# Optimization experiments

Hardware: AMD Instinct MI355X
Metric: run time of the kernel (lower is better)

## Reference

```python
import jax, jax.numpy as jnp
import numpy as np
from jax import lax

SCALES = [0.5, 0.25, 0.125, 0.0625]
D_MODEL = 256
IN_CH = 1


def setup_inputs() -> dict:
    key = jax.random.key(0)
    ks = jax.random.split(key, 16)
    x = jax.random.normal(ks[0], (2, D_MODEL, 256, 256), dtype=jnp.float32)
    m = jax.random.uniform(ks[1], (2, IN_CH, 256, 256), dtype=jnp.float32)
    s = 0.05
    Wq = jax.random.normal(ks[2], (D_MODEL, D_MODEL, 1, 1), jnp.float32) * s
    bq = jax.random.normal(ks[3], (D_MODEL,), jnp.float32) * s
    Wk = jax.random.normal(ks[4], (D_MODEL, D_MODEL, 1, 1), jnp.float32) * s
    bk = jax.random.normal(ks[5], (D_MODEL,), jnp.float32) * s
    Wv = jax.random.normal(ks[6], (D_MODEL, D_MODEL, 1, 1), jnp.float32) * s
    bv = jax.random.normal(ks[7], (D_MODEL,), jnp.float32) * s
    Wmq = jax.random.normal(ks[8], (D_MODEL, IN_CH, 1, 1), jnp.float32) * s
    bmq = jax.random.normal(ks[9], (D_MODEL,), jnp.float32) * s
    Wmk = jax.random.normal(ks[10], (D_MODEL, IN_CH, 1, 1), jnp.float32) * s
    bmk = jax.random.normal(ks[11], (D_MODEL,), jnp.float32) * s
    Wo = jax.random.normal(ks[12], (D_MODEL, D_MODEL, 3, 3), jnp.float32) * s
    bo = jax.random.normal(ks[13], (D_MODEL,), jnp.float32) * s
    return {"x": x, "m": m, "Wq": Wq, "bq": bq, "Wk": Wk, "bk": bk,
            "Wv": Wv, "bv": bv, "Wmq": Wmq, "bmq": bmq, "Wmk": Wmk, "bmk": bmk,
            "Wo": Wo, "bo": bo, "b": 1, "c": 256}


def _conv1x1(z, W, bias):
    # W: (O, I, 1, 1)
    return jnp.einsum('bihw,oi->bohw', z, W[:, :, 0, 0]) + bias[None, :, None, None]


def _forward(x, m, Wq, bq, Wk, bk, Wv, bv, Wmq, bmq, Wmk, bmk, Wo, bo, b, c):
    bt, _, h, w = x.shape  # h, w are multiples of 64 -> pad is zero
    t = bt // b
    n_scales = len(SCALES)
    d_k = c // n_scales

    q = _conv1x1(x, Wq, bq)
    k = _conv1x1(x, Wk, bk)
    v = _conv1x1(x, Wv, bv)
    mq = _conv1x1(m, Wmq, bmq)
    mk = _conv1x1(m, Wmk, bmk)

    outs = []
    for i, scale in enumerate(SCALES):
        height, width = int(h * scale), int(w * scale)
        out_h, out_w = h // height, w // width
        sl = slice(i * d_k, (i + 1) * d_k)

        def patch(z):
            # (b, t, d_k, out_h, height, out_w, width) -> (b, t*out_h*out_w, d_k*height*width)
            z = z[:, sl].reshape(b, t, d_k, out_h, height, out_w, width)
            z = z.transpose(0, 1, 3, 5, 2, 4, 6)
            return z.reshape(b, t * out_h * out_w, d_k * height * width)

        Q, K, V = patch(q), patch(k), patch(v)
        MQ, MK = patch(mq), patch(mk)
        inv_sqrt_d = 1.0 / jnp.sqrt(jnp.asarray(Q.shape[-1], jnp.float32))
        scores = jnp.einsum('bnd,bmd->bnm', Q, K) * inv_sqrt_d
        mask_scores = jnp.einsum('bnd,bmd->bnm', MQ, MK) * inv_sqrt_d
        p_attn = jax.nn.softmax(scores * mask_scores, axis=-1)
        y = jnp.einsum('bnm,bmd->bnd', p_attn, V)
        # back to (bt, d_k, h, w)
        y = y.reshape(b, t, out_h, out_w, d_k, height, width)
        y = y.transpose(0, 1, 4, 2, 5, 3, 6).reshape(bt, d_k, h, w)
        outs.append(y)

    out = jnp.concatenate(outs, axis=1)
    z = lax.conv_general_dilated(out, Wo, window_strides=(1, 1),
                                 padding=((1, 1), (1, 1)),
                                 dimension_numbers=('NCHW', 'OIHW', 'NCHW'))
    z = z + bo[None, :, None, None]
    return jnp.where(z > 0, z, 0.2 * z)  # LeakyReLU(0.2)


def reference(x, m, Wq, bq, Wk, bk, Wv, bv, Wmq, bmq, Wmk, bmk, Wo, bo, b, c):
    return _forward(x, m, Wq, bq, Wk, bk, Wv, bv, Wmq, bmq, Wmk, bmk, Wo, bo, b, c)
```

## Files before the change

kernel.cpp:

```cpp
#include <hip/hip_runtime.h>
#include <stdint.h>


typedef __attribute__((ext_vector_type(8))) short short8;
typedef __attribute__((ext_vector_type(4))) float floatx4;
typedef __attribute__((ext_vector_type(4))) unsigned int uintx4;

#define DEV static __device__ __forceinline__

DEV unsigned short f2bf(float f) {
  unsigned u = __builtin_bit_cast(unsigned, f);
  unsigned r = u + 0x7FFFu + ((u >> 16) & 1u);
  return (unsigned short)(r >> 16);
}

DEV void patch_row(int n, int sc, int lw, int& pt, int& sp0) {
  pt = n >> (2 + 2 * sc);
  int rem = n & ((4 << (2 * sc)) - 1);
  int oh = rem >> (1 + sc), ow = rem & ((2 << sc) - 1);
  sp0 = (oh << (lw + 8)) + (ow << lw);
}

__global__ void k_prep_w(const float* __restrict__ Wq, const float* __restrict__ Wk,
                         const float* __restrict__ Wv, const float* __restrict__ bq,
                         const float* __restrict__ bk, const float* __restrict__ bv,
                         const float* __restrict__ Wmq, const float* __restrict__ bmq,
                         const float* __restrict__ Wmk, const float* __restrict__ bmk,
                         unsigned short* __restrict__ wqkv, float* __restrict__ bias,
                         float* __restrict__ msc) {
  int b = blockIdx.x;
  int t = threadIdx.x;
  if (b < 768) {
    const float* src = b < 256 ? (Wq + b * 256) : (b < 512 ? (Wk + (b - 256) * 256)
                                                           : (Wv + (b - 512) * 256));
    wqkv[b * 256 + t] = f2bf(src[t]);
    if (t == 0) bias[b] = b < 256 ? bq[b] : (b < 512 ? bk[b - 256] : bv[b - 512]);
  } else {
    int sc = t >> 6, lane = t & 63;
    int ch = sc * 64 + lane;
    float a0 = Wmq[ch] * Wmk[ch];
    float a1 = Wmq[ch] * bmk[ch];
    float a2 = bmq[ch] * Wmk[ch];
    float a3 = bmq[ch] * bmk[ch];
    for (int off = 32; off; off >>= 1) {
      a0 += __shfl_xor(a0, off); a1 += __shfl_xor(a1, off);
      a2 += __shfl_xor(a2, off); a3 += __shfl_xor(a3, off);
    }
    if (lane == 0) {
      msc[sc * 4 + 0] = a0; msc[sc * 4 + 1] = a1;
      msc[sc * 4 + 2] = a2; msc[sc * 4 + 3] = a3;
    }
  }
}

__global__ void k_prep_wo(const float* __restrict__ Wo, unsigned short* __restrict__ wobf,
                          float* __restrict__ scoresG, unsigned int* __restrict__ pbuf) {
  int blk = blockIdx.x;
  if (blk < 2304) {
    int didx = blk >> 8, o = blk & 255, c = threadIdx.x;
    wobf[didx * 65536 + o * 256 + c] = f2bf(Wo[o * 2304 + c * 9 + didx]);
  } else {
    int i = (blk - 2304) * 256 + threadIdx.x;
    if (i < 559232) scoresG[i] = 0.f;
    if (i < 140032) pbuf[i] = 0u;
  }
}

__global__ __launch_bounds__(256) void k_xt(const float* __restrict__ x,
                                            unsigned short* __restrict__ xt) {
  __shared__ __align__(16) unsigned short tile[64][72];
  int p0 = blockIdx.x * 64, c0 = blockIdx.y * 64, t = blockIdx.z;
  int tid = threadIdx.x;
  {
    int cc = tid >> 2, pq = (tid & 3) * 16;
    const float* src = x + ((t * 256 + c0 + cc) * 65536 + p0 + pq);
    __align__(16) unsigned short tmp[16];
#pragma unroll
    for (int e = 0; e < 16; e += 4) {
      floatx4 v = *(const floatx4*)(src + e);
      tmp[e + 0] = f2bf(v[0]); tmp[e + 1] = f2bf(v[1]);
      tmp[e + 2] = f2bf(v[2]); tmp[e + 3] = f2bf(v[3]);
    }
    *(uintx4*)&tile[cc][pq] = *(const uintx4*)&tmp[0];
    *(uintx4*)&tile[cc][pq + 8] = *(const uintx4*)&tmp[8];
  }
  __syncthreads();
  {
    int pp = tid >> 2, cg = (tid & 3) * 16;
    __align__(16) unsigned short outv[16];
#pragma unroll
    for (int e = 0; e < 16; ++e) outv[e] = tile[cg + e][pp];
    unsigned short* dst = xt + ((t * 65536 + p0 + pp) * 256 + c0 + cg);
    *(uintx4*)dst = *(const uintx4*)&outv[0];
    *(uintx4*)(dst + 8) = *(const uintx4*)&outv[8];
  }
}

__global__ __launch_bounds__(256) void k_yt(const unsigned short* __restrict__ ynat,
                                            unsigned short* __restrict__ yt) {
  __shared__ __align__(16) unsigned short tile[64][72];
  int p0 = blockIdx.x * 64, c0 = blockIdx.y * 64, t = blockIdx.z;
  int tid = threadIdx.x;
  {
    int cc = tid >> 2, pq = (tid & 3) * 16;
    const unsigned short* src = ynat + ((t * 256 + c0 + cc) * 65536 + p0 + pq);
    *(uintx4*)&tile[cc][pq] = *(const uintx4*)src;
    *(uintx4*)&tile[cc][pq + 8] = *(const uintx4*)(src + 8);
  }
  __syncthreads();
  {
    int pp = tid >> 2, cg = (tid & 3) * 16;
    __align__(16) unsigned short outv[16];
#pragma unroll
    for (int e = 0; e < 16; ++e) outv[e] = tile[cg + e][pp];
    unsigned short* dst = yt + ((t * 65536 + p0 + pp) * 256 + c0 + cg);
    *(uintx4*)dst = *(const uintx4*)&outv[0];
    *(uintx4*)(dst + 8) = *(const uintx4*)&outv[8];
  }
}

__global__ __launch_bounds__(256, 2) void k_qkv(const unsigned short* __restrict__ xt,
                                                const unsigned short* __restrict__ wqkv,
                                                const float* __restrict__ bias,
                                                unsigned short* __restrict__ qkv) {
  extern __shared__ __align__(16) char smem[];
  auto As = (unsigned short (*)[64])(smem);
  auto Bs = (unsigned short (*)[64])(smem + 16384);
  auto Cs = (unsigned short (*)[280])(smem);
  int flat = blockIdx.x;
  int lg = (flat & 7) * 384 + (flat >> 3);
  int n_t = lg / 6, m_t = lg - n_t * 6;
  int n0 = n_t << 8, m0 = m_t << 7;
  int tid = threadIdx.x;
  int w = tid >> 6, l = tid & 63;
  int wr = w >> 1, wc = w & 1;
  int l15 = l & 15, lhi = l >> 4;
  int sr = tid >> 1, sbase = (tid & 1) * 4, r7 = sr & 7;
  int b7 = tid & 7;
  const unsigned short* gA = wqkv + (m0 + sr) * 256 + sbase * 8;
  const unsigned short* gB = xt + (n0 + tid) * 256;
  floatx4 zf = {0.f, 0.f, 0.f, 0.f};
  floatx4 acc[4][8];
#pragma unroll
  for (int i = 0; i < 4; ++i)
#pragma unroll
    for (int j = 0; j < 8; ++j) acc[i][j] = zf;
  uintx4 ra[4], rb[8];
#define QLOAD(K0) { const uintx4* pa = (const uintx4*)(gA + (K0)); \
                    ra[0] = pa[0]; ra[1] = pa[1]; ra[2] = pa[2]; ra[3] = pa[3]; \
                    const uintx4* pb = (const uintx4*)(gB + (K0)); \
                    rb[0] = pb[0]; rb[1] = pb[1]; rb[2] = pb[2]; rb[3] = pb[3]; \
                    rb[4] = pb[4]; rb[5] = pb[5]; rb[6] = pb[6]; rb[7] = pb[7]; }
  QLOAD(0);
#pragma unroll
  for (int ch = 0; ch < 4; ++ch) {
    __syncthreads();
#pragma unroll
    for (int j = 0; j < 4; ++j)
      *(uintx4*)&As[sr][((sbase + j) ^ r7) * 8] = ra[j];
#pragma unroll
    for (int j = 0; j < 8; ++j)
      *(uintx4*)&Bs[tid][(j ^ b7) * 8] = rb[j];
    __syncthreads();
    if (ch < 3) QLOAD((ch + 1) * 64);
#pragma unroll
    for (int kk = 0; kk < 2; ++kk) {
      short8 af[4];
#pragma unroll
      for (int f = 0; f < 4; ++f) {
        int arow = wr * 64 + f * 16 + l15;
        af[f] = *(const short8*)&As[arow][(((kk << 2) + lhi) ^ (arow & 7)) * 8];
      }
#pragma unroll
      for (int fn = 0; fn < 8; ++fn) {
        int brow = wc * 128 + fn * 16 + l15;
        short8 b = *(const short8*)&Bs[brow][(((kk << 2) + lhi) ^ (brow & 7)) * 8];
#pragma unroll
        for (int fm = 0; fm < 4; ++fm)
          acc[fm][fn] = __builtin_amdgcn_mfma_f32_16x16x32_bf16(af[fm], b, acc[fm][fn], 0, 0, 0);
      }
    }
  }
#undef QLOAD
#pragma unroll
  for (int h = 0; h < 2; ++h) {
    __syncthreads();
    if (wr == h) {
#pragma unroll
      for (int fm = 0; fm < 4; ++fm) {
#pragma unroll
        for (int rr = 0; rr < 4; ++rr) {
          int rl = fm * 16 + lhi * 4 + rr;
          float bv = bias[m0 + h * 64 + rl];
#pragma unroll
          for (int fn = 0; fn < 8; ++fn)
            Cs[rl][wc * 128 + fn * 16 + l15] = f2bf(acc[fm][fn][rr] + bv);
        }
      }
    }
    __syncthreads();
    {
      int p8 = (tid & 31) * 8;
      int pcol = n0 + p8;
      int t = pcol >> 16, p = pcol & 65535;
#pragma unroll
      for (int pass = 0; pass < 8; ++pass) {
        int rl = (tid >> 5) + pass * 8;
        uintx4 v = *(const uintx4*)&Cs[rl][p8];
        *(uintx4*)&qkv[((t * 768 + m0 + h * 64 + rl) << 16) + p] = v;
      }
    }
  }
}

__global__ __launch_bounds__(256) void k_gram2(const float* __restrict__ m,
                                               float* __restrict__ G) {
  __shared__ __align__(16) float Ns[32][68];
  __shared__ __align__(16) float Ms[32][68];
  int bid = blockIdx.x;
  int sc, tn, tm, z, nchunks, soff;
  if (bid < 32)      { sc = 0; tn = 0; tm = 0; z = bid;      nchunks = 8; soff = 0; }
  else if (bid < 40) { sc = 1; tn = 0; tm = 0; z = bid - 32; nchunks = 8; soff = 64; }
  else if (bid < 72) { int r = bid - 40; int tl = r >> 1; sc = 2; tn = tl >> 2; tm = tl & 3; z = r & 1; nchunks = 8; soff = 1088; }
  else               { int tl = bid - 72; sc = 3; tn = tl >> 4; tm = tl & 15; z = 0; nchunks = 4; soff = 17472; }
  int lw = 7 - sc, W = 1 << lw, N = 8 << (2 * sc);
  int kbase = z * nchunks * 64;
  int n0 = tn * 32, m0 = tm * 32;
  int tid = threadIdx.x;
  bool isA = tid < 128;
  int u = tid & 127;
  int srow = u >> 2, sslot0 = (u & 3) * 4;
  int grow = (isA ? n0 : m0) + srow;
  bool valid = grow < N;
  int pt = 0, sp0 = 0;
  if (valid) patch_row(grow, sc, lw, pt, sp0);
  int gbase = pt * 65536 + sp0;
  int trc = tid >> 4, tcc = tid & 15;
  float a00 = 0.f, a01 = 0.f, a10 = 0.f, a11 = 0.f;
  floatx4 zf = {0.f, 0.f, 0.f, 0.f};
  for (int c = 0; c < nchunks; ++c) {
    int k0 = kbase + c * 64;
    floatx4 v[4];
#pragma unroll
    for (int j = 0; j < 4; ++j) {
      v[j] = zf;
      if (valid) {
        int s = k0 + (sslot0 + j) * 4;
        int hh = s >> lw, ww = s & (W - 1);
        v[j] = *(const floatx4*)(m + gbase + (hh << 8) + ww);
      }
    }
    __syncthreads();
    float* dstrow = isA ? &Ns[srow][0] : &Ms[srow][0];
#pragma unroll
    for (int j = 0; j < 4; ++j) *(floatx4*)&dstrow[(sslot0 + j) * 4] = v[j];
    __syncthreads();
#pragma unroll 4
    for (int k = 0; k < 64; k += 4) {
      floatx4 na = *(const floatx4*)&Ns[2 * trc][k];
      floatx4 nb = *(const floatx4*)&Ns[2 * trc + 1][k];
      floatx4 ma = *(const floatx4*)&Ms[2 * tcc][k];
      floatx4 mb = *(const floatx4*)&Ms[2 * tcc + 1][k];
#pragma unroll
      for (int e = 0; e < 4; ++e) {
        a00 += na[e] * ma[e]; a01 += na[e] * mb[e];
        a10 += nb[e] * ma[e]; a11 += nb[e] * mb[e];
      }
    }
  }
  int rn = n0 + 2 * trc, rm = m0 + 2 * tcc;
  float res[2][2] = {{a00, a01}, {a10, a11}};
#pragma unroll
  for (int i = 0; i < 2; ++i)
#pragma unroll
    for (int j = 0; j < 2; ++j) {
      if (rn + i < N && rm + j < N) {
        float* dst = &G[soff + (rn + i) * N + rm + j];
        if (sc < 3) atomicAdd(dst, res[i][j]); else *dst = res[i][j];
      }
    }
}

__global__ void k_rsum(const float* __restrict__ m, float* __restrict__ rbuf) {
  int row = blockIdx.x, lane = threadIdx.x;
  int sc, n;
  if (row < 8)        { sc = 0; n = row; }
  else if (row < 40)  { sc = 1; n = row - 8; }
  else if (row < 168) { sc = 2; n = row - 40; }
  else                { sc = 3; n = row - 168; }
  int lw = 7 - sc, W = 1 << lw;
  int pt, sp0;
  patch_row(n, sc, lw, pt, sp0);
  int base = pt * 65536 + sp0;
  int S = 1 << (14 - 2 * sc);
  float acc = 0.f;
  for (int s = lane; s < S; s += 64) {
    int hh = s >> lw, ww = s & (W - 1);
    acc += m[base + (hh << 8) + ww];
  }
  for (int off = 32; off; off >>= 1) acc += __shfl_xor(acc, off);
  if (lane == 0) rbuf[row] = acc;
}

__global__ __launch_bounds__(256) void k_scores2(const unsigned short* __restrict__ qkv,
                                                 float* __restrict__ scores) {
  __shared__ __align__(16) unsigned short As[32][136];
  __shared__ __align__(16) unsigned short Bs[32][136];
  int bid = blockIdx.x;
  int sc, tn, tm, z, soff;
  if (bid < 256)      { sc = 0; tn = 0; tm = 0; z = bid;       soff = 0; }
  else                { sc = 1; tn = 0; tm = 0; z = bid - 256; soff = 64; }
  int lw = 7 - sc, W = 1 << lw, lS = 14 - 2 * sc, N = 8 << (2 * sc);
  int n0 = tn * 32, m0 = tm * 32;
  int kbase = z * 4096;
  int tid = threadIdx.x, w = tid >> 6, l = tid & 63;
  int wr = w >> 1, wc = w & 1, l15 = l & 15, lhi = l >> 4;
  floatx4 acc = {0.f, 0.f, 0.f, 0.f};
  bool isA = tid < 128;
  int u = tid & 127;
  int srow = u >> 2, sslot0 = (u & 3) * 4;
  int grow = (isA ? n0 : m0) + srow;
  int cb = (isA ? 0 : 256) + sc * 64;
  int pt = 0, sp0 = 0;
  bool valid = grow < N;
  if (valid) patch_row(grow, sc, lw, pt, sp0);
  int rowbase = (pt * 768 + cb) * 65536 + sp0;
  uintx4 zu = {0u, 0u, 0u, 0u};
  uintx4 r[4];
#define SLOAD(KS) { int kb2 = kbase + (KS) * 128; \
  _Pragma("unroll") for (int j = 0; j < 4; ++j) { \
    uintx4 v = zu; \
    if (valid) { int k = kb2 + (sslot0 + j) * 8; \
      int cl = k >> lS; int s = k & ((1 << lS) - 1); \
      int hh = s >> lw, ww = s & (W - 1); \
      v = *(const uintx4*)(qkv + rowbase + cl * 65536 + (hh << 8) + ww); } \
    r[j] = v; } }
  SLOAD(0);
  for (int ks = 0; ks < 32; ++ks) {
    __syncthreads();
    {
      unsigned short* dstrow = isA ? &As[srow][0] : &Bs[srow][0];
#pragma unroll
      for (int j = 0; j < 4; ++j) *(uintx4*)&dstrow[(sslot0 + j) * 8] = r[j];
    }
    __syncthreads();
    if (ks < 31) SLOAD(ks + 1);
#pragma unroll
    for (int kk = 0; kk < 4; ++kk) {
      short8 a = *(const short8*)&As[wr * 16 + l15][(kk * 4 + lhi) * 8];
      short8 b = *(const short8*)&Bs[wc * 16 + l15][(kk * 4 + lhi) * 8];
      acc = __builtin_amdgcn_mfma_f32_16x16x32_bf16(a, b, acc, 0, 0, 0);
    }
  }
#undef SLOAD
  int rrow = n0 + wr * 16 + lhi * 4;
  int ccol = m0 + wc * 16 + l15;
  if (ccol < N) {
#pragma unroll
    for (int rr = 0; rr < 4; ++rr)
      if (rrow + rr < N) atomicAdd(&scores[soff + (rrow + rr) * N + ccol], acc[rr]);
  }
}

__global__ __launch_bounds__(256) void k_scores_big(const unsigned short* __restrict__ qkv,
                                                    float* __restrict__ scores) {
  __shared__ __align__(16) unsigned short As[128][64];
  __shared__ __align__(16) unsigned short Bs[128][64];
  int flat = blockIdx.x;
  int lg = (flat & 7) * 20 + (flat >> 3);
  int sc, tn, tm, z, soff;
  if (lg < 32) { sc = 2; tn = 0; tm = 0; z = lg; soff = 1088; }
  else { int r = lg - 32; int tl = r >> 3; sc = 3; tn = tl >> 2; tm = tl & 3; z = r & 7; soff = 17472; }
  int N = 8 << (2 * sc);
  int lw = 7 - sc, W = 1 << lw, lS = 14 - 2 * sc;
  int n0 = tn * 128, m0 = tm * 128;
  int kbase = z * 2048;
  int tid = threadIdx.x;
  int w = tid >> 6, l = tid & 63;
  int wr = w >> 1, wc = w & 1;
  int l15 = l & 15, lhi = l >> 4;
  int sr = tid >> 1, sbase = (tid & 1) * 4, r7 = sr & 7;
  int ptA, spA, ptB, spB;
  patch_row(n0 + sr, sc, lw, ptA, spA);
  patch_row(m0 + sr, sc, lw, ptB, spB);
  int baseA = (ptA * 768 + sc * 64) * 65536 + spA;
  int baseB = (ptB * 768 + 256 + sc * 64) * 65536 + spB;
  floatx4 zf = {0.f, 0.f, 0.f, 0.f};
  floatx4 acc[4][4];
#pragma unroll
  for (int i = 0; i < 4; ++i)
#pragma unroll
    for (int j = 0; j < 4; ++j) acc[i][j] = zf;
  uintx4 ra[4], rb[4];
#define GLOAD(K0) { \
  _Pragma("unroll") for (int j = 0; j < 4; ++j) { \
    int k = kbase + (K0) + (sbase + j) * 8; \
    int cl = k >> lS; int s = k & ((1 << lS) - 1); \
    int hh = s >> lw, ww = s & (W - 1); \
    int off = cl * 65536 + (hh << 8) + ww; \
    ra[j] = *(const uintx4*)(qkv + baseA + off); \
    rb[j] = *(const uintx4*)(qkv + baseB + off); } }
  GLOAD(0);
  for (int st = 0; st < 32; ++st) {
    __syncthreads();
#pragma unroll
    for (int j = 0; j < 4; ++j) {
      *(uintx4*)&As[sr][((sbase + j) ^ r7) * 8] = ra[j];
      *(uintx4*)&Bs[sr][((sbase + j) ^ r7) * 8] = rb[j];
    }
    __syncthreads();
    if (st < 31) GLOAD((st + 1) * 64);
#pragma unroll
    for (int kk = 0; kk < 2; ++kk) {
      short8 af[4], bfr[4];
#pragma unroll
      for (int f = 0; f < 4; ++f) {
        int arow = wr * 64 + f * 16 + l15;
        af[f] = *(const short8*)&As[arow][(((kk << 2) + lhi) ^ (arow & 7)) * 8];
        int brow = wc * 64 + f * 16 + l15;
        bfr[f] = *(const short8*)&Bs[brow][(((kk << 2) + lhi) ^ (brow & 7)) * 8];
      }
#pragma unroll
      for (int fm = 0; fm < 4; ++fm)
#pragma unroll
        for (int fn = 0; fn < 4; ++fn)
          acc[fm][fn] = __builtin_amdgcn_mfma_f32_16x16x32_bf16(af[fm], bfr[fn], acc[fm][fn], 0, 0, 0);
    }
  }
#undef GLOAD
#pragma unroll
  for (int fm = 0; fm < 4; ++fm) {
    int nrow = n0 + wr * 64 + fm * 16 + lhi * 4;
#pragma unroll
    for (int rr = 0; rr < 4; ++rr) {
#pragma unroll
      for (int fn = 0; fn < 4; ++fn) {
        int mcol = m0 + wc * 64 + fn * 16 + l15;
        atomicAdd(&scores[soff + (nrow + rr) * N + mcol], acc[fm][fn][rr]);
      }
    }
  }
}

__global__ void k_softmax(const float* __restrict__ scores, const float* __restrict__ G,
                          const float* __restrict__ rbuf, const float* __restrict__ msc,
                          unsigned short* __restrict__ pbuf) {
  int row = blockIdx.x, lane = threadIdx.x;
  int sc, n, roff, soff, poff;
  if (row < 8)        { sc = 0; n = row;       roff = 0;   soff = 0;     poff = 0; }
  else if (row < 40)  { sc = 1; n = row - 8;   roff = 8;   soff = 64;    poff = 512; }
  else if (row < 168) { sc = 2; n = row - 40;  roff = 40;  soff = 1088;  poff = 1536; }
  else                { sc = 3; n = row - 168; roff = 168; soff = 17472; poff = 17920; }
  int N = 8 << (2 * sc);
  int Kpad = (sc < 2) ? 32 : N;
  float Sf = (float)(1 << (14 - 2 * sc));
  float invD = 1.0f / (float)(1 << (20 - 2 * sc));
  float alpha = msc[sc * 4 + 0], beta = msc[sc * 4 + 1];
  float gamma = msc[sc * 4 + 2], delta = msc[sc * 4 + 3];
  float rn = rbuf[roff + n];
  float vals[8];
  float mx = -1e30f;
#pragma unroll
  for (int j = 0; j < 8; ++j) {
    float v = -1e30f;
    int mcol = lane + j * 64;
    if (j * 64 < N && mcol < N) {
      float sq = scores[soff + n * N + mcol];
      float g = G[soff + n * N + mcol];
      float rm = rbuf[roff + mcol];
      v = sq * (alpha * g + beta * rn + gamma * rm + delta * Sf) * invD;
    }
    vals[j] = v;
    mx = fmaxf(mx, v);
  }
  for (int off = 32; off; off >>= 1) mx = fmaxf(mx, __shfl_xor(mx, off));
  float sum = 0.f;
#pragma unroll
  for (int j = 0; j < 8; ++j) {
    int mcol = lane + j * 64;
    float e = 0.f;
    if (j * 64 < N && mcol < N) e = __expf(vals[j] - mx);
    vals[j] = e;
    sum += e;
  }
  for (int off = 32; off; off >>= 1) sum += __shfl_xor(sum, off);
  float inv = 1.f / sum;
#pragma unroll
  for (int j = 0; j < 8; ++j) {
    int mcol = lane + j * 64;
    if (j * 64 < N && mcol < N) pbuf[poff + n * Kpad + mcol] = f2bf(vals[j] * inv);
  }
}

__global__ __launch_bounds__(256) void k_pv(const unsigned short* __restrict__ qkv,
                                            const unsigned short* __restrict__ pbuf,
                                            unsigned short* __restrict__ ynat) {
  int bid = blockIdx.x;
  int sc, bx, by;
  if (bid < 4096)      { sc = 0; bx = bid; by = 0; }
  else if (bid < 6144) { sc = 1; bx = bid - 4096; by = 0; }
  else if (bid < 8192) { int r = bid - 6144; sc = 2; bx = r >> 1; by = r & 1; }
  else                 { int r = bid - 8192; sc = 3; bx = r >> 3; by = r & 7; }
  int WR    = (sc == 0) ? 1 : (sc == 1) ? 2 : 4;
  int logWC = (sc == 0) ? 2 : (sc == 1) ? 1 : 0;
  int poff  = (sc == 0) ? 0 : (sc == 1) ? 512 : (sc == 2) ? 1536 : 17920;
  int lw = 7 - sc, W = 1 << lw;
  int lS = 14 - 2 * sc;
  int N = 8 << (2 * sc);
  int Kpad = (sc < 2) ? 32 : N;
  int WC = 1 << logWC;
  int d0 = bx * (WC * 64);
  int nb = by * (WR * 16);
  __shared__ __align__(16) unsigned short As[2][64][40];
  __shared__ __align__(16) unsigned short Bt[2][256][32];
  int tid = threadIdx.x;
  int w = tid >> 6, l = tid & 63;
  int wr = w >> logWC, wc = w & (WC - 1);
  int l15 = l & 15, lhi = l >> 4;
  floatx4 zf = {0.f, 0.f, 0.f, 0.f};
  floatx4 acc[4];
#pragma unroll
  for (int i = 0; i < 4; ++i) acc[i] = zf;
  int bmp = tid & 15;
  int dg = tid >> 4;
  bool act0 = (WC > 1) || (dg < 8);
  bool has1 = (WC == 4);
  bool doA = tid < WR * 64;
  int arow = tid >> 2, akg = (tid & 3) * 8;
  int ksteps = Kpad >> 5;
  uintx4 zu = {0u, 0u, 0u, 0u};
  int vcb = (512 + sc * 64) * 65536;
  uintx4 av = zu, lo0 = zu, hi0 = zu, lo1 = zu, hi1 = zu;
#define PLOADS(KS) { int k0 = (KS) * 32; \
    av = zu; lo0 = zu; hi0 = zu; lo1 = zu; hi1 = zu; \
    if (doA) av = *(const uintx4*)(pbuf + poff + (nb + arow) * Kpad + k0 + akg); \
    int gm0 = k0 + 2 * bmp, gm1 = gm0 + 1; \
    bool mv0 = gm0 < N, mv1 = gm1 < N; \
    int pt0 = 0, sp00 = 0, pt1 = 0, sp01 = 0; \
    if (mv0) patch_row(gm0, sc, lw, pt0, sp00); \
    if (mv1) patch_row(gm1, sc, lw, pt1, sp01); \
    { int d = d0 + dg * 8; int cl = d >> lS; int s = d & ((1 << lS) - 1); \
      int hh = s >> lw, ww = s & (W - 1); int sp = (hh << 8) + ww; \
      if (act0 && mv0) lo0 = *(const uintx4*)(qkv + pt0 * 768 * 65536 + vcb + cl * 65536 + sp00 + sp); \
      if (act0 && mv1) hi0 = *(const uintx4*)(qkv + pt1 * 768 * 65536 + vcb + cl * 65536 + sp01 + sp); } \
    if (has1) { int d = d0 + (dg + 16) * 8; int cl = d >> lS; int s = d & ((1 << lS) - 1); \
      int hh = s >> lw, ww = s & (W - 1); int sp = (hh << 8) + ww; \
      if (mv0) lo1 = *(const uintx4*)(qkv + pt0 * 768 * 65536 + vcb + cl * 65536 + sp00 + sp); \
      if (mv1) hi1 = *(const uintx4*)(qkv + pt1 * 768 * 65536 + vcb + cl * 65536 + sp01 + sp); } }
  PLOADS(0);
  for (int ks = 0; ks < ksteps; ++ks) {
    int b = ks & 1;
    if (doA) *(uintx4*)&As[b][arow][akg] = av;
    if (act0) {
      int du = dg * 8;
#pragma unroll
      for (int j = 0; j < 8; ++j) {
        int d = du + j;
        unsigned losh = (lo0[j >> 1] >> ((j & 1) * 16)) & 0xFFFFu;
        unsigned hish = (hi0[j >> 1] >> ((j & 1) * 16)) & 0xFFFFu;
        unsigned wv = losh | (hish << 16);
        int slot = (bmp >> 2) ^ ((d >> 1) & 3) ^ ((d >> 3) & 3);
        ((unsigned int*)&Bt[b][d][0])[slot * 4 + (bmp & 3)] = wv;
      }
    }
    if (has1) {
      int du = (dg + 16) * 8;
#pragma unroll
      for (int j = 0; j < 8; ++j) {
        int d = du + j;
        unsigned losh = (lo1[j >> 1] >> ((j & 1) * 16)) & 0xFFFFu;
        unsigned hish = (hi1[j >> 1] >> ((j & 1) * 16)) & 0xFFFFu;
        unsigned wv = losh | (hish << 16);
        int slot = (bmp >> 2) ^ ((d >> 1) & 3) ^ ((d >> 3) & 3);
        ((unsigned int*)&Bt[b][d][0])[slot * 4 + (bmp & 3)] = wv;
      }
    }
    __syncthreads();
    if (ks + 1 < ksteps) PLOADS(ks + 1);
    short8 a = *(const short8*)&As[b][wr * 16 + l15][lhi * 8];
#pragma unroll
    for (int fn = 0; fn < 4; ++fn) {
      int row = wc * 64 + fn * 16 + l15;
      int slot = lhi ^ ((row >> 1) & 3) ^ ((row >> 3) & 3);
      short8 bb = *(const short8*)&Bt[b][row][slot * 8];
      acc[fn] = __builtin_amdgcn_mfma_f32_16x16x32_bf16(a, bb, acc[fn], 0, 0, 0);
    }
  }
#undef PLOADS
  int nrow = nb + wr * 16 + lhi * 4;
#pragma unroll
  for (int rr = 0; rr < 4; ++rr) {
    int n = nrow + rr;
    if (n < N) {
      int pt, sp0;
      patch_row(n, sc, lw, pt, sp0);
#pragma unroll
      for (int fn = 0; fn < 4; ++fn) {
        int d = d0 + wc * 64 + fn * 16 + l15;
        int cl = d >> lS;
        int s = d & ((1 << lS) - 1);
        int hh = s >> lw, ww = s & (W - 1);
        int c = sc * 64 + cl;
        ynat[(pt * 256 + c) * 65536 + sp0 + (hh << 8) + ww] = f2bf(acc[fn][rr]);
      }
    }
  }
}

__global__ __launch_bounds__(256, 2) void k_conv(const unsigned short* __restrict__ yt,
                                                 const unsigned short* __restrict__ wo,
                                                 const float* __restrict__ bo,
                                                 float* __restrict__ out) {
  __shared__ __align__(16) unsigned short As[128][128];
  __shared__ __align__(16) unsigned short Bs[130][64];
  int flat = blockIdx.x;
  int lg = ((flat & 7) << 7) + (flat >> 3);
  int n_t = lg >> 1, m_t = lg & 1;
  int n0 = n_t << 8, m0 = m_t << 7;
  int tt = n0 >> 16, yy = (n0 >> 8) & 255;
  int tid = threadIdx.x;
  int w = tid >> 6, l = tid & 63;
  int wr = w >> 1, wc = w & 1;
  int l15 = l & 15, lhi = l >> 4;
  int a_d0 = tid >> 7, a_o0 = tid & 127;
  bool doA1 = tid < 128;
  bool doBh = tid >= 254;
  floatx4 zf = {0.f, 0.f, 0.f, 0.f};
  floatx4 acc[4][8];
#pragma unroll
  for (int i = 0; i < 4; ++i)
#pragma unroll
    for (int j = 0; j < 8; ++j) acc[i][j] = zf;
  uintx4 zu = {0u, 0u, 0u, 0u};
  uintx4 rb[4], ra0[4], ra1[4];
  const unsigned short* ybase = yt + (tt << 24);
#define CLOAD(ST) { \
    int dy = (ST) >> 3, cc = ((ST) & 7) << 5; \
    int yq = yy + dy - 1; \
    bool yv = (unsigned)yq < 256u; \
    { int xq = tid - 1; \
      if (yv && (unsigned)xq < 256u) { \
        const uintx4* p = (const uintx4*)(ybase + ((yq << 8) + xq) * 256 + cc); \
        rb[0] = p[0]; rb[1] = p[1]; rb[2] = p[2]; rb[3] = p[3]; \
      } else { rb[0] = zu; rb[1] = zu; rb[2] = zu; rb[3] = zu; } } \
    { const uintx4* p = (const uintx4*)(wo + (dy * 3 + a_d0) * 65536 + (m0 + a_o0) * 256 + cc); \
      ra0[0] = p[0]; ra0[1] = p[1]; ra0[2] = p[2]; ra0[3] = p[3]; } \
    if (doA1) { \
      const uintx4* p = (const uintx4*)(wo + (dy * 3 + 2) * 65536 + (m0 + tid) * 256 + cc); \
      ra1[0] = p[0]; ra1[1] = p[1]; ra1[2] = p[2]; ra1[3] = p[3]; \
    } else if (doBh) { \
      int xq = tid + 1; \
      if (yv && xq < 256) { \
        const uintx4* p = (const uintx4*)(ybase + ((yq << 8) + xq) * 256 + cc); \
        ra1[0] = p[0]; ra1[1] = p[1]; ra1[2] = p[2]; ra1[3] = p[3]; \
      } else { ra1[0] = zu; ra1[1] = zu; ra1[2] = zu; ra1[3] = zu; } } }
  CLOAD(0);
  for (int st = 0; st < 24; ++st) {
    __syncthreads();
    {
      int brow = tid >> 1, bhf = (tid & 1) * 4, br7 = brow & 7;
#pragma unroll
      for (int j = 0; j < 4; ++j)
        *(uintx4*)&Bs[brow][((bhf + j) ^ br7) * 8] = rb[j];
      int ao7 = a_o0 & 7;
#pragma unroll
      for (int j = 0; j < 4; ++j)
        *(uintx4*)&As[a_o0][((a_d0 * 4 + j) ^ ao7) * 8] = ra0[j];
      if (doA1) {
        int o7 = tid & 7;
#pragma unroll
        for (int j = 0; j < 4; ++j)
          *(uintx4*)&As[tid][((8 + j) ^ o7) * 8] = ra1[j];
      } else if (doBh) {
        int xh = tid + 2;
        int brow2 = xh >> 1, bhf2 = (xh & 1) * 4, br72 = brow2 & 7;
#pragma unroll
        for (int j = 0; j < 4; ++j)
          *(uintx4*)&Bs[brow2][((bhf2 + j) ^ br72) * 8] = ra1[j];
      }
    }
    __syncthreads();
    if (st < 23) CLOAD(st + 1);
#pragma unroll
    for (int dx = 0; dx < 3; ++dx) {
      short8 af[4];
#pragma unroll
      for (int f = 0; f < 4; ++f) {
        int ol = wr * 64 + f * 16 + l15;
        af[f] = *(const short8*)&As[ol][((dx * 4 + lhi) ^ (ol & 7)) * 8];
      }
#pragma unroll
      for (int fn = 0; fn < 8; ++fn) {
        int xh = wc * 128 + fn * 16 + l15 + dx;
        short8 b = *(const short8*)&Bs[xh >> 1][((((xh & 1) * 4 + lhi)) ^ ((xh >> 1) & 7)) * 8];
#pragma unroll
        for (int fm = 0; fm < 4; ++fm)
          acc[fm][fn] = __builtin_amdgcn_mfma_f32_16x16x32_bf16(af[fm], b, acc[fm][fn], 0, 0, 0);
      }
    }
  }
#undef CLOAD
#pragma unroll
  for (int fm = 0; fm < 4; ++fm) {
    int o = m0 + wr * 64 + fm * 16 + lhi * 4;
#pragma unroll
    for (int rr = 0; rr < 4; ++rr) {
      float bias = bo[o + rr];
#pragma unroll
      for (int fn = 0; fn < 8; ++fn) {
        int xcol = wc * 128 + fn * 16 + l15;
        float z = acc[fm][fn][rr] + bias;
        out[((tt * 256 + o + rr) << 16) + (yy << 8) + xcol] = z > 0.f ? z : 0.2f * z;
      }
    }
  }
}

extern "C" void kernel_launch(void* const* d_in, const int* in_sizes, int n_in,
                              void* d_out, int out_size, void* d_ws, size_t ws_size,
                              hipStream_t stream) {
  const float* x   = (const float*)d_in[0];
  const float* m   = (const float*)d_in[1];
  const float* Wq  = (const float*)d_in[2];
  const float* bq  = (const float*)d_in[3];
  const float* Wk  = (const float*)d_in[4];
  const float* bk  = (const float*)d_in[5];
  const float* Wv  = (const float*)d_in[6];
  const float* bv  = (const float*)d_in[7];
  const float* Wmq = (const float*)d_in[8];
  const float* bmq = (const float*)d_in[9];
  const float* Wmk = (const float*)d_in[10];
  const float* bmk = (const float*)d_in[11];
  const float* Wo  = (const float*)d_in[12];
  const float* bo  = (const float*)d_in[13];

  char* ws = (char*)d_ws;
  unsigned short* qkv   = (unsigned short*)(ws);
  unsigned short* xtb   = (unsigned short*)(ws + 201326592);
  unsigned short* wqkv  = (unsigned short*)(ws + 268435456);
  unsigned short* wobf  = (unsigned short*)(ws + 268828672);
  float* bias           = (float*)(ws + 270008320);
  float* msc            = (float*)(ws + 270011392);
  float* scores         = (float*)(ws + 270011456);
  float* G              = (float*)(ws + 271129920);
  float* rbuf           = (float*)(ws + 272248384);
  unsigned short* pbuf  = (unsigned short*)(ws + 272251104);
  float* out            = (float*)d_out;
  unsigned short* ynat  = (unsigned short*)d_out;

  k_prep_w<<<dim3(769), dim3(256), 0, stream>>>(Wq, Wk, Wv, bq, bk, bv, Wmq, bmq, Wmk, bmk,
                                                wqkv, bias, msc);
  k_prep_wo<<<dim3(4489), dim3(256), 0, stream>>>(Wo, wobf, scores, (unsigned int*)pbuf);
  k_xt<<<dim3(1024, 4, 2), dim3(256), 0, stream>>>(x, xtb);
  k_qkv<<<dim3(3072), dim3(256), 49152, stream>>>(xtb, wqkv, bias, qkv);
  k_gram2<<<dim3(328), dim3(256), 0, stream>>>(m, G);
  k_rsum<<<dim3(680), dim3(64), 0, stream>>>(m, rbuf);
  k_scores2<<<dim3(320), dim3(256), 0, stream>>>(qkv, scores);
  k_scores_big<<<dim3(160), dim3(256), 0, stream>>>(qkv, scores);
  k_softmax<<<dim3(680), dim3(64), 0, stream>>>(scores, G, rbuf, msc, pbuf);
  k_pv<<<dim3(10240), dim3(256), 0, stream>>>(qkv, pbuf, ynat);
  k_yt<<<dim3(1024, 4, 2), dim3(256), 0, stream>>>(ynat, xtb);
  k_conv<<<dim3(1024), dim3(256), 0, stream>>>(xtb, wobf, bo, out);
}
```

Baseline: 583.7 us.

## Merge small kernels and retile 3x3 conv to 64-channel blocks

Merges the two weight-prep kernels into one launch, the mask Gram and row-sum kernels into one, and the small and big score kernels into one. Each merge removes a launch and lets independent blocks run together. The 3x3 output conv now computes a 64-output-channel by 256-pixel tile per block instead of 128x256, with half the accumulators, smaller shared memory, a 3-blocks-per-SM bound and twice the blocks. This trades more occupancy for re-reading the activation tile once per extra channel block.

```diff
diff --git a/kernel.cpp b/kernel.cpp
--- a/kernel.cpp
+++ b/kernel.cpp
@@ -21,21 +21,25 @@
   sp0 = (oh << (lw + 8)) + (ow << lw);
 }
 
-__global__ void k_prep_w(const float* __restrict__ Wq, const float* __restrict__ Wk,
-                         const float* __restrict__ Wv, const float* __restrict__ bq,
-                         const float* __restrict__ bk, const float* __restrict__ bv,
-                         const float* __restrict__ Wmq, const float* __restrict__ bmq,
-                         const float* __restrict__ Wmk, const float* __restrict__ bmk,
-                         unsigned short* __restrict__ wqkv, float* __restrict__ bias,
-                         float* __restrict__ msc) {
-  int b = blockIdx.x;
+__global__ void k_prep(const float* __restrict__ Wq, const float* __restrict__ Wk,
+                       const float* __restrict__ Wv, const float* __restrict__ bq,
+                       const float* __restrict__ bk, const float* __restrict__ bv,
+                       const float* __restrict__ Wmq, const float* __restrict__ bmq,
+                       const float* __restrict__ Wmk, const float* __restrict__ bmk,
+                       const float* __restrict__ Wo, const float* __restrict__ bo,
+                       unsigned short* __restrict__ wqkv, float* __restrict__ bias,
+                       float* __restrict__ msc, unsigned short* __restrict__ wobf,
+                       float* __restrict__ scoresG, unsigned int* __restrict__ pbuf) {
+  int bid = blockIdx.x;
   int t = threadIdx.x;
-  if (b < 768) {
-    const float* src = b < 256 ? (Wq + b * 256) : (b < 512 ? (Wk + (b - 256) * 256)
-                                                           : (Wv + (b - 512) * 256));
-    wqkv[b * 256 + t] = f2bf(src[t]);
-    if (t == 0) bias[b] = b < 256 ? bq[b] : (b < 512 ? bk[b - 256] : bv[b - 512]);
-  } else {
+  if (bid < 768) {
+    const float* src = bid < 256 ? (Wq + bid * 256) : (bid < 512 ? (Wk + (bid - 256) * 256)
+                                                                 : (Wv + (bid - 512) * 256));
+    wqkv[bid * 256 + t] = f2bf(src[t]);
+    if (t == 0) bias[bid] = bid < 256 ? bq[bid] : (bid < 512 ? bk[bid - 256] : bv[bid - 512]);
+    return;
+  }
+  if (bid == 768) {
     int sc = t >> 6, lane = t & 63;
     int ch = sc * 64 + lane;
     float a0 = Wmq[ch] * Wmk[ch];
@@ -50,17 +54,14 @@
       msc[sc * 4 + 0] = a0; msc[sc * 4 + 1] = a1;
       msc[sc * 4 + 2] = a2; msc[sc * 4 + 3] = a3;
     }
-  }
-}
-
-__global__ void k_prep_wo(const float* __restrict__ Wo, unsigned short* __restrict__ wobf,
-                          float* __restrict__ scoresG, unsigned int* __restrict__ pbuf) {
-  int blk = blockIdx.x;
+    return;
+  }
+  int blk = bid - 769;
   if (blk < 2304) {
-    int didx = blk >> 8, o = blk & 255, c = threadIdx.x;
+    int didx = blk >> 8, o = blk & 255, c = t;
     wobf[didx * 65536 + o * 256 + c] = f2bf(Wo[o * 2304 + c * 9 + didx]);
   } else {
-    int i = (blk - 2304) * 256 + threadIdx.x;
+    int i = (blk - 2304) * 256 + t;
     if (i < 559232) scoresG[i] = 0.f;
     if (i < 140032) pbuf[i] = 0u;
   }
@@ -213,11 +214,37 @@
   }
 }
 
-__global__ __launch_bounds__(256) void k_gram2(const float* __restrict__ m,
-                                               float* __restrict__ G) {
+__global__ __launch_bounds__(256) void k_mask(const float* __restrict__ m,
+                                              float* __restrict__ G,
+                                              float* __restrict__ rbuf) {
+  int bid = blockIdx.x;
+  int tid = threadIdx.x;
+  if (bid >= 328) {
+    int row = (bid - 328) * 4 + (tid >> 6);
+    int lane = tid & 63;
+    if (row < 680) {
+      int sc, n;
+      if (row < 8)        { sc = 0; n = row; }
+      else if (row < 40)  { sc = 1; n = row - 8; }
+      else if (row < 168) { sc = 2; n = row - 40; }
+      else                { sc = 3; n = row - 168; }
+      int lw = 7 - sc, W = 1 << lw;
+      int pt, sp0;
+      patch_row(n, sc, lw, pt, sp0);
+      int base = pt * 65536 + sp0;
+      int S = 1 << (14 - 2 * sc);
+      float acc = 0.f;
+      for (int s = lane; s < S; s += 64) {
+        int hh = s >> lw, ww = s & (W - 1);
+        acc += m[base + (hh << 8) + ww];
+      }
+      for (int off = 32; off; off >>= 1) acc += __shfl_xor(acc, off);
+      if (lane == 0) rbuf[row] = acc;
+    }
+    return;
+  }
   __shared__ __align__(16) float Ns[32][68];
   __shared__ __align__(16) float Ms[32][68];
-  int bid = blockIdx.x;
   int sc, tn, tm, z, nchunks, soff;
   if (bid < 32)      { sc = 0; tn = 0; tm = 0; z = bid;      nchunks = 8; soff = 0; }
   else if (bid < 40) { sc = 1; tn = 0; tm = 0; z = bid - 32; nchunks = 8; soff = 64; }
@@ -226,7 +253,6 @@
   int lw = 7 - sc, W = 1 << lw, N = 8 << (2 * sc);
   int kbase = z * nchunks * 64;
   int n0 = tn * 32, m0 = tm * 32;
-  int tid = threadIdx.x;
   bool isA = tid < 128;
   int u = tid & 127;
   int srow = u >> 2, sslot0 = (u & 3) * 4;
@@ -281,52 +307,108 @@
     }
 }
 
-__global__ void k_rsum(const float* __restrict__ m, float* __restrict__ rbuf) {
-  int row = blockIdx.x, lane = threadIdx.x;
-  int sc, n;
-  if (row < 8)        { sc = 0; n = row; }
-  else if (row < 40)  { sc = 1; n = row - 8; }
-  else if (row < 168) { sc = 2; n = row - 40; }
-  else                { sc = 3; n = row - 168; }
-  int lw = 7 - sc, W = 1 << lw;
-  int pt, sp0;
-  patch_row(n, sc, lw, pt, sp0);
-  int base = pt * 65536 + sp0;
-  int S = 1 << (14 - 2 * sc);
-  float acc = 0.f;
-  for (int s = lane; s < S; s += 64) {
-    int hh = s >> lw, ww = s & (W - 1);
-    acc += m[base + (hh << 8) + ww];
-  }
-  for (int off = 32; off; off >>= 1) acc += __shfl_xor(acc, off);
-  if (lane == 0) rbuf[row] = acc;
-}
-
-__global__ __launch_bounds__(256) void k_scores2(const unsigned short* __restrict__ qkv,
-                                                 float* __restrict__ scores) {
-  __shared__ __align__(16) unsigned short As[32][136];
-  __shared__ __align__(16) unsigned short Bs[32][136];
+__global__ __launch_bounds__(256) void k_scores_all(const unsigned short* __restrict__ qkv,
+                                                    float* __restrict__ scores) {
+  __shared__ __align__(16) char sbuf[32768];
   int bid = blockIdx.x;
-  int sc, tn, tm, z, soff;
-  if (bid < 256)      { sc = 0; tn = 0; tm = 0; z = bid;       soff = 0; }
-  else                { sc = 1; tn = 0; tm = 0; z = bid - 256; soff = 64; }
-  int lw = 7 - sc, W = 1 << lw, lS = 14 - 2 * sc, N = 8 << (2 * sc);
-  int n0 = tn * 32, m0 = tm * 32;
-  int kbase = z * 4096;
-  int tid = threadIdx.x, w = tid >> 6, l = tid & 63;
+  int tid = threadIdx.x;
+  int w = tid >> 6, l = tid & 63;
   int wr = w >> 1, wc = w & 1, l15 = l & 15, lhi = l >> 4;
-  floatx4 acc = {0.f, 0.f, 0.f, 0.f};
-  bool isA = tid < 128;
-  int u = tid & 127;
-  int srow = u >> 2, sslot0 = (u & 3) * 4;
-  int grow = (isA ? n0 : m0) + srow;
-  int cb = (isA ? 0 : 256) + sc * 64;
-  int pt = 0, sp0 = 0;
-  bool valid = grow < N;
-  if (valid) patch_row(grow, sc, lw, pt, sp0);
-  int rowbase = (pt * 768 + cb) * 65536 + sp0;
   uintx4 zu = {0u, 0u, 0u, 0u};
-  uintx4 r[4];
+  floatx4 zf = {0.f, 0.f, 0.f, 0.f};
+  if (bid < 160) {
+    auto As = (unsigned short (*)[64])(sbuf);
+    auto Bs = (unsigned short (*)[64])(sbuf + 16384);
+    int lg = (bid & 7) * 20 + (bid >> 3);
+    int sc, tn, tm, z, soff;
+    if (lg < 32) { sc = 2; tn = 0; tm = 0; z = lg; soff = 1088; }
+    else { int r = lg - 32; int tl = r >> 3; sc = 3; tn = tl >> 2; tm = tl & 3; z = r & 7; soff = 17472; }
+    int N = 8 << (2 * sc);
+    int lw = 7 - sc, W = 1 << lw, lS = 14 - 2 * sc;
+    int n0 = tn * 128, m0 = tm * 128;
+    int kbase = z * 2048;
+    int sr = tid >> 1, sbase = (tid & 1) * 4, r7 = sr & 7;
+    int ptA, spA, ptB, spB;
+    patch_row(n0 + sr, sc, lw, ptA, spA);
+    patch_row(m0 + sr, sc, lw, ptB, spB);
+    int baseA = (ptA * 768 + sc * 64) * 65536 + spA;
+    int baseB = (ptB * 768 + 256 + sc * 64) * 65536 + spB;
+    floatx4 acc[4][4];
+#pragma unroll
+    for (int i = 0; i < 4; ++i)
+#pragma unroll
+      for (int j = 0; j < 4; ++j) acc[i][j] = zf;
+    uintx4 ra[4], rb[4];
+#define GLOAD(K0) { \
+  _Pragma("unroll") for (int j = 0; j < 4; ++j) { \
+    int k = kbase + (K0) + (sbase + j) * 8; \
+    int cl = k >> lS; int s = k & ((1 << lS) - 1); \
+    int hh = s >> lw, ww = s & (W - 1); \
+    int off = cl * 65536 + (hh << 8) + ww; \
+    ra[j] = *(const uintx4*)(qkv + baseA + off); \
+    rb[j] = *(const uintx4*)(qkv + baseB + off); } }
+    GLOAD(0);
+    for (int st = 0; st < 32; ++st) {
+      __syncthreads();
+#pragma unroll
+      for (int j = 0; j < 4; ++j) {
+        *(uintx4*)&As[sr][((sbase + j) ^ r7) * 8] = ra[j];
+        *(uintx4*)&Bs[sr][((sbase + j) ^ r7) * 8] = rb[j];
+      }
+      __syncthreads();
+      if (st < 31) GLOAD((st + 1) * 64);
+#pragma unroll
+      for (int kk = 0; kk < 2; ++kk) {
+        short8 af[4], bfr[4];
+#pragma unroll
+        for (int f = 0; f < 4; ++f) {
+          int arow = wr * 64 + f * 16 + l15;
+          af[f] = *(const short8*)&As[arow][(((kk << 2) + lhi) ^ (arow & 7)) * 8];
+          int brow = wc * 64 + f * 16 + l15;
+          bfr[f] = *(const short8*)&Bs[brow][(((kk << 2) + lhi) ^ (brow & 7)) * 8];
+        }
+#pragma unroll
+        for (int fm = 0; fm < 4; ++fm)
+#pragma unroll
+          for (int fn = 0; fn < 4; ++fn)
+            acc[fm][fn] = __builtin_amdgcn_mfma_f32_16x16x32_bf16(af[fm], bfr[fn], acc[fm][fn], 0, 0, 0);
+      }
+    }
+#undef GLOAD
+#pragma unroll
+    for (int fm = 0; fm < 4; ++fm) {
+      int nrow = n0 + wr * 64 + fm * 16 + lhi * 4;
+#pragma unroll
+      for (int rr = 0; rr < 4; ++rr) {
+#pragma unroll
+        for (int fn = 0; fn < 4; ++fn) {
+          int mcol = m0 + wc * 64 + fn * 16 + l15;
+          atomicAdd(&scores[soff + (nrow + rr) * N + mcol], acc[fm][fn][rr]);
+        }
+      }
+    }
+    return;
+  }
+  {
+    auto As = (unsigned short (*)[136])(sbuf);
+    auto Bs = (unsigned short (*)[136])(sbuf + 8704);
+    int b2 = bid - 160;
+    int sc, z, soff;
+    if (b2 < 256) { sc = 0; z = b2;       soff = 0; }
+    else          { sc = 1; z = b2 - 256; soff = 64; }
+    int lw = 7 - sc, W = 1 << lw, lS = 14 - 2 * sc, N = 8 << (2 * sc);
+    int kbase = z * 4096;
+    floatx4 acc = zf;
+    bool isA = tid < 128;
+    int u = tid & 127;
+    int srow = u >> 2, sslot0 = (u & 3) * 4;
+    int grow = srow;
+    int cb = (isA ? 0 : 256) + sc * 64;
+    int pt = 0, sp0 = 0;
+    bool valid = grow < N;
+    if (valid) patch_row(grow, sc, lw, pt, sp0);
+    int rowbase = (pt * 768 + cb) * 65536 + sp0;
+    uintx4 r[4];
 #define SLOAD(KS) { int kb2 = kbase + (KS) * 128; \
   _Pragma("unroll") for (int j = 0; j < 4; ++j) { \
     uintx4 v = zu; \
@@ -335,109 +417,30 @@
       int hh = s >> lw, ww = s & (W - 1); \
       v = *(const uintx4*)(qkv + rowbase + cl * 65536 + (hh << 8) + ww); } \
     r[j] = v; } }
-  SLOAD(0);
-  for (int ks = 0; ks < 32; ++ks) {
-    __syncthreads();
-    {
-      unsigned short* dstrow = isA ? &As[srow][0] : &Bs[srow][0];
-#pragma unroll
-      for (int j = 0; j < 4; ++j) *(uintx4*)&dstrow[(sslot0 + j) * 8] = r[j];
-    }
-    __syncthreads();
-    if (ks < 31) SLOAD(ks + 1);
-#pragma unroll
-    for (int kk = 0; kk < 4; ++kk) {
-      short8 a = *(const short8*)&As[wr * 16 + l15][(kk * 4 + lhi) * 8];
-      short8 b = *(const short8*)&Bs[wc * 16 + l15][(kk * 4 + lhi) * 8];
-      acc = __builtin_amdgcn_mfma_f32_16x16x32_bf16(a, b, acc, 0, 0, 0);
-    }
-  }
+    SLOAD(0);
+    for (int ks = 0; ks < 32; ++ks) {
+      __syncthreads();
+      {
+        unsigned short* dstrow = isA ? &As[srow][0] : &Bs[srow][0];
+#pragma unroll
+        for (int j = 0; j < 4; ++j) *(uintx4*)&dstrow[(sslot0 + j) * 8] = r[j];
+      }
+      __syncthreads();
+      if (ks < 31) SLOAD(ks + 1);
+#pragma unroll
+      for (int kk = 0; kk < 4; ++kk) {
+        short8 a = *(const short8*)&As[wr * 16 + l15][(kk * 4 + lhi) * 8];
+        short8 b = *(const short8*)&Bs[wc * 16 + l15][(kk * 4 + lhi) * 8];
+        acc = __builtin_amdgcn_mfma_f32_16x16x32_bf16(a, b, acc, 0, 0, 0);
+      }
+    }
 #undef SLOAD
-  int rrow = n0 + wr * 16 + lhi * 4;
-  int ccol = m0 + wc * 16 + l15;
-  if (ccol < N) {
-#pragma unroll
-    for (int rr = 0; rr < 4; ++rr)
-      if (rrow + rr < N) atomicAdd(&scores[soff + (rrow + rr) * N + ccol], acc[rr]);
-  }
-}
-
-__global__ __launch_bounds__(256) void k_scores_big(const unsigned short* __restrict__ qkv,
-                                                    float* __restrict__ scores) {
-  __shared__ __align__(16) unsigned short As[128][64];
-  __shared__ __align__(16) unsigned short Bs[128][64];
-  int flat = blockIdx.x;
-  int lg = (flat & 7) * 20 + (flat >> 3);
-  int sc, tn, tm, z, soff;
-  if (lg < 32) { sc = 2; tn = 0; tm = 0; z = lg; soff = 1088; }
-  else { int r = lg - 32; int tl = r >> 3; sc = 3; tn = tl >> 2; tm = tl & 3; z = r & 7; soff = 17472; }
-  int N = 8 << (2 * sc);
-  int lw = 7 - sc, W = 1 << lw, lS = 14 - 2 * sc;
-  int n0 = tn * 128, m0 = tm * 128;
-  int kbase = z * 2048;
-  int tid = threadIdx.x;
-  int w = tid >> 6, l = tid & 63;
-  int wr = w >> 1, wc = w & 1;
-  int l15 = l & 15, lhi = l >> 4;
-  int sr = tid >> 1, sbase = (tid & 1) * 4, r7 = sr & 7;
-  int ptA, spA, ptB, spB;
-  patch_row(n0 + sr, sc, lw, ptA, spA);
-  patch_row(m0 + sr, sc, lw, ptB, spB);
-  int baseA = (ptA * 768 + sc * 64) * 65536 + spA;
-  int baseB = (ptB * 768 + 256 + sc * 64) * 65536 + spB;
-  floatx4 zf = {0.f, 0.f, 0.f, 0.f};
-  floatx4 acc[4][4];
-#pragma unroll
-  for (int i = 0; i < 4; ++i)
-#pragma unroll
-    for (int j = 0; j < 4; ++j) acc[i][j] = zf;
-  uintx4 ra[4], rb[4];
-#define GLOAD(K0) { \
-  _Pragma("unroll") for (int j = 0; j < 4; ++j) { \
-    int k = kbase + (K0) + (sbase + j) * 8; \
-    int cl = k >> lS; int s = k & ((1 << lS) - 1); \
-    int hh = s >> lw, ww = s & (W - 1); \
-    int off = cl * 65536 + (hh << 8) + ww; \
-    ra[j] = *(const uintx4*)(qkv + baseA + off); \
-    rb[j] = *(const uintx4*)(qkv + baseB + off); } }
-  GLOAD(0);
-  for (int st = 0; st < 32; ++st) {
-    __syncthreads();
-#pragma unroll
-    for (int j = 0; j < 4; ++j) {
-      *(uintx4*)&As[sr][((sbase + j) ^ r7) * 8] = ra[j];
-      *(uintx4*)&Bs[sr][((sbase + j) ^ r7) * 8] = rb[j];
-    }
-    __syncthreads();
-    if (st < 31) GLOAD((st + 1) * 64);
-#pragma unroll
-    for (int kk = 0; kk < 2; ++kk) {
-      short8 af[4], bfr[4];
-#pragma unroll
-      for (int f = 0; f < 4; ++f) {
-        int arow = wr * 64 + f * 16 + l15;
-        af[f] = *(const short8*)&As[arow][(((kk << 2) + lhi) ^ (arow & 7)) * 8];
-        int brow = wc * 64 + f * 16 + l15;
-        bfr[f] = *(const short8*)&Bs[brow][(((kk << 2) + lhi) ^ (brow & 7)) * 8];
-      }
-#pragma unroll
-      for (int fm = 0; fm < 4; ++fm)
-#pragma unroll
-        for (int fn = 0; fn < 4; ++fn)
-          acc[fm][fn] = __builtin_amdgcn_mfma_f32_16x16x32_bf16(af[fm], bfr[fn], acc[fm][fn], 0, 0, 0);
-    }
-  }
-#undef GLOAD
-#pragma unroll
-  for (int fm = 0; fm < 4; ++fm) {
-    int nrow = n0 + wr * 64 + fm * 16 + lhi * 4;
-#pragma unroll
-    for (int rr = 0; rr < 4; ++rr) {
-#pragma unroll
-      for (int fn = 0; fn < 4; ++fn) {
-        int mcol = m0 + wc * 64 + fn * 16 + l15;
-        atomicAdd(&scores[soff + (nrow + rr) * N + mcol], acc[fm][fn][rr]);
-      }
+    int rrow = wr * 16 + lhi * 4;
+    int ccol = wc * 16 + l15;
+    if (ccol < N) {
+#pragma unroll
+      for (int rr = 0; rr < 4; ++rr)
+        if (rrow + rr < N) atomicAdd(&scores[soff + (rrow + rr) * N + ccol], acc[rr]);
     }
   }
 }
@@ -607,32 +610,31 @@
   }
 }
 
-__global__ __launch_bounds__(256, 2) void k_conv(const unsigned short* __restrict__ yt,
+__global__ __launch_bounds__(256, 3) void k_conv(const unsigned short* __restrict__ yt,
                                                  const unsigned short* __restrict__ wo,
                                                  const float* __restrict__ bo,
                                                  float* __restrict__ out) {
-  __shared__ __align__(16) unsigned short As[128][128];
+  __shared__ __align__(16) unsigned short As[64][128];
   __shared__ __align__(16) unsigned short Bs[130][64];
   int flat = blockIdx.x;
-  int lg = ((flat & 7) << 7) + (flat >> 3);
-  int n_t = lg >> 1, m_t = lg & 1;
-  int n0 = n_t << 8, m0 = m_t << 7;
+  int lg = ((flat & 7) << 8) + (flat >> 3);
+  int n_t = lg >> 2, m_t = lg & 3;
+  int n0 = n_t << 8, m0 = m_t << 6;
   int tt = n0 >> 16, yy = (n0 >> 8) & 255;
   int tid = threadIdx.x;
   int w = tid >> 6, l = tid & 63;
-  int wr = w >> 1, wc = w & 1;
   int l15 = l & 15, lhi = l >> 4;
-  int a_d0 = tid >> 7, a_o0 = tid & 127;
-  bool doA1 = tid < 128;
+  bool doA = tid < 192;
+  int a_dx = tid >> 6, a_o = tid & 63;
   bool doBh = tid >= 254;
   floatx4 zf = {0.f, 0.f, 0.f, 0.f};
-  floatx4 acc[4][8];
+  floatx4 acc[4][4];
 #pragma unroll
   for (int i = 0; i < 4; ++i)
 #pragma unroll
-    for (int j = 0; j < 8; ++j) acc[i][j] = zf;
+    for (int j = 0; j < 4; ++j) acc[i][j] = zf;
   uintx4 zu = {0u, 0u, 0u, 0u};
-  uintx4 rb[4], ra0[4], ra1[4];
+  uintx4 rb[4], ra[4], rh[4];
   const unsigned short* ybase = yt + (tt << 24);
 #define CLOAD(ST) { \
     int dy = (ST) >> 3, cc = ((ST) & 7) << 5; \
@@ -643,17 +645,15 @@
         const uintx4* p = (const uintx4*)(ybase + ((yq << 8) + xq) * 256 + cc); \
         rb[0] = p[0]; rb[1] = p[1]; rb[2] = p[2]; rb[3] = p[3]; \
       } else { rb[0] = zu; rb[1] = zu; rb[2] = zu; rb[3] = zu; } } \
-    { const uintx4* p = (const uintx4*)(wo + (dy * 3 + a_d0) * 65536 + (m0 + a_o0) * 256 + cc); \
-      ra0[0] = p[0]; ra0[1] = p[1]; ra0[2] = p[2]; ra0[3] = p[3]; } \
-    if (doA1) { \
-      const uintx4* p = (const uintx4*)(wo + (dy * 3 + 2) * 65536 + (m0 + tid) * 256 + cc); \
-      ra1[0] = p[0]; ra1[1] = p[1]; ra1[2] = p[2]; ra1[3] = p[3]; \
+    if (doA) { \
+      const uintx4* p = (const uintx4*)(wo + (dy * 3 + a_dx) * 65536 + (m0 + a_o) * 256 + cc); \
+      ra[0] = p[0]; ra[1] = p[1]; ra[2] = p[2]; ra[3] = p[3]; \
     } else if (doBh) { \
-      int xq = tid + 1; \
+      int xq = tid + 1;   \
       if (yv && xq < 256) { \
         const uintx4* p = (const uintx4*)(ybase + ((yq << 8) + xq) * 256 + cc); \
-        ra1[0] = p[0]; ra1[1] = p[1]; ra1[2] = p[2]; ra1[3] = p[3]; \
-      } else { ra1[0] = zu; ra1[1] = zu; ra1[2] = zu; ra1[3] = zu; } } }
+        rh[0] = p[0]; rh[1] = p[1]; rh[2] = p[2]; rh[3] = p[3]; \
+      } else { rh[0] = zu; rh[1] = zu; rh[2] = zu; rh[3] = zu; } } }
   CLOAD(0);
   for (int st = 0; st < 24; ++st) {
     __syncthreads();
@@ -662,21 +662,17 @@
 #pragma unroll
       for (int j = 0; j < 4; ++j)
         *(uintx4*)&Bs[brow][((bhf + j) ^ br7) * 8] = rb[j];
-      int ao7 = a_o0 & 7;
-#pragma unroll
-      for (int j = 0; j < 4; ++j)
-        *(uintx4*)&As[a_o0][((a_d0 * 4 + j) ^ ao7) * 8] = ra0[j];
-      if (doA1) {
-        int o7 = tid & 7;
+      if (doA) {
+        int o7 = a_o & 7;
 #pragma unroll
         for (int j = 0; j < 4; ++j)
-          *(uintx4*)&As[tid][((8 + j) ^ o7) * 8] = ra1[j];
+          *(uintx4*)&As[a_o][((a_dx * 4 + j) ^ o7) * 8] = ra[j];
       } else if (doBh) {
         int xh = tid + 2;
         int brow2 = xh >> 1, bhf2 = (xh & 1) * 4, br72 = brow2 & 7;
 #pragma unroll
         for (int j = 0; j < 4; ++j)
-          *(uintx4*)&Bs[brow2][((bhf2 + j) ^ br72) * 8] = ra1[j];
+          *(uintx4*)&Bs[brow2][((bhf2 + j) ^ br72) * 8] = rh[j];
       }
     }
     __syncthreads();
@@ -686,12 +682,12 @@
       short8 af[4];
 #pragma unroll
       for (int f = 0; f < 4; ++f) {
-        int ol = wr * 64 + f * 16 + l15;
+        int ol = f * 16 + l15;
         af[f] = *(const short8*)&As[ol][((dx * 4 + lhi) ^ (ol & 7)) * 8];
       }
 #pragma unroll
-      for (int fn = 0; fn < 8; ++fn) {
-        int xh = wc * 128 + fn * 16 + l15 + dx;
+      for (int fn = 0; fn < 4; ++fn) {
+        int xh = w * 64 + fn * 16 + l15 + dx;
         short8 b = *(const short8*)&Bs[xh >> 1][((((xh & 1) * 4 + lhi)) ^ ((xh >> 1) & 7)) * 8];
 #pragma unroll
         for (int fm = 0; fm < 4; ++fm)
@@ -702,13 +698,13 @@
 #undef CLOAD
 #pragma unroll
   for (int fm = 0; fm < 4; ++fm) {
-    int o = m0 + wr * 64 + fm * 16 + lhi * 4;
+    int o = m0 + fm * 16 + lhi * 4;
 #pragma unroll
     for (int rr = 0; rr < 4; ++rr) {
       float bias = bo[o + rr];
 #pragma unroll
-      for (int fn = 0; fn < 8; ++fn) {
-        int xcol = wc * 128 + fn * 16 + l15;
+      for (int fn = 0; fn < 4; ++fn) {
+        int xcol = w * 64 + fn * 16 + l15;
         float z = acc[fm][fn][rr] + bias;
         out[((tt * 256 + o + rr) << 16) + (yy << 8) + xcol] = z > 0.f ? z : 0.2f * z;
       }
@@ -748,17 +744,15 @@
   float* out            = (float*)d_out;
   unsigned short* ynat  = (unsigned short*)d_out;
 
-  k_prep_w<<<dim3(769), dim3(256), 0, stream>>>(Wq, Wk, Wv, bq, bk, bv, Wmq, bmq, Wmk, bmk,
-                                                wqkv, bias, msc);
-  k_prep_wo<<<dim3(4489), dim3(256), 0, stream>>>(Wo, wobf, scores, (unsigned int*)pbuf);
+  k_prep<<<dim3(5258), dim3(256), 0, stream>>>(Wq, Wk, Wv, bq, bk, bv, Wmq, bmq, Wmk, bmk,
+                                               Wo, bo, wqkv, bias, msc, wobf, scores,
+                                               (unsigned int*)pbuf);
   k_xt<<<dim3(1024, 4, 2), dim3(256), 0, stream>>>(x, xtb);
   k_qkv<<<dim3(3072), dim3(256), 49152, stream>>>(xtb, wqkv, bias, qkv);
-  k_gram2<<<dim3(328), dim3(256), 0, stream>>>(m, G);
-  k_rsum<<<dim3(680), dim3(64), 0, stream>>>(m, rbuf);
-  k_scores2<<<dim3(320), dim3(256), 0, stream>>>(qkv, scores);
-  k_scores_big<<<dim3(160), dim3(256), 0, stream>>>(qkv, scores);
+  k_mask<<<dim3(498), dim3(256), 0, stream>>>(m, G, rbuf);
+  k_scores_all<<<dim3(480), dim3(256), 0, stream>>>(qkv, scores);
   k_softmax<<<dim3(680), dim3(64), 0, stream>>>(scores, G, rbuf, msc, pbuf);
   k_pv<<<dim3(10240), dim3(256), 0, stream>>>(qkv, pbuf, ynat);
   k_yt<<<dim3(1024, 4, 2), dim3(256), 0, stream>>>(ynat, xtb);
-  k_conv<<<dim3(1024), dim3(256), 0, stream>>>(xtb, wobf, bo, out);
-}
+  k_conv<<<dim3(2048), dim3(256), 0, stream>>>(xtb, wobf, bo, out);
+}
```

Measured after the change: 576.4 us. No clear change (-1.2%).
